# Optimization experiments

Hardware: AMD Instinct MI355X
Metric: run time of the kernel (lower is better)

The kernel has to match this reference:

```python
import jax, jax.numpy as jnp
import numpy as np

# --- module hyperparameters (init_kwargs) ---
IN_CH = 512
OUT_CH = 512
NUM_HEADS = 8
MODES = 64
LQ = 4096
LKV = 4096
E = IN_CH // NUM_HEADS      # per-head input dim = 64
EO = OUT_CH // NUM_HEADS    # per-head output dim = 64
B = 16

# mode_select_method='lowest' -> lowest-frequency modes, sorted (deterministic)
INDEX_Q = np.arange(min(MODES, LQ // 2))    # [Mq]
INDEX_KV = np.arange(min(MODES, LKV // 2))  # [Mkv]
SCALE = 1.0 / (IN_CH * OUT_CH)


def setup_inputs() -> dict:
    key = jax.random.key(0)
    kq, kk, kv, kw1, kw2 = jax.random.split(key, 5)
    return {
        "q": jax.random.normal(kq, (B, LQ, NUM_HEADS, E), jnp.float32),
        "k": jax.random.normal(kk, (B, LKV, NUM_HEADS, E), jnp.float32),
        "v": jax.random.normal(kv, (B, LKV, NUM_HEADS, E), jnp.float32),
        "weights1": SCALE * jax.random.normal(kw1, (NUM_HEADS, E, EO, len(INDEX_Q)), jnp.float32),
        "weights2": SCALE * jax.random.normal(kw2, (NUM_HEADS, E, EO, len(INDEX_Q)), jnp.float32),
    }


def reference(q, k, v, weights1, weights2):
    # q: [B, Lq, H, E]; k, v: [B, Lkv, H, E] (v is computed-but-unused in the
    # original forward; kept for signature fidelity).
    Bq, Lq, H, _ = q.shape
    xq = jnp.transpose(q, (0, 2, 3, 1))  # [B, H, E, Lq]
    xk = jnp.transpose(k, (0, 2, 3, 1))  # [B, H, E, Lkv]

    # rFFT along time, then gather the selected frequency modes
    xq_ft = jnp.fft.rfft(xq, axis=-1)[..., INDEX_Q]    # [B, H, E, Mq] complex
    xk_ft = jnp.fft.rfft(xk, axis=-1)[..., INDEX_KV]   # [B, H, E, Mkv] complex

    # complex cross-attention over modes (contract head-dim E)
    xqk = jnp.einsum('bhex,bhey->bhxy', xq_ft, xk_ft)  # [B, H, Mq, Mkv]
    # tanh applied independently to real/imag parts (as in compl activation)
    xqk = jax.lax.complex(jnp.tanh(xqk.real), jnp.tanh(xqk.imag))

    xqkv = jnp.einsum('bhxy,bhey->bhex', xqk, xk_ft)   # [B, H, E, Mq]

    w = jax.lax.complex(weights1, weights2)            # [H, E, EO, Mq]
    xqkvw = jnp.einsum('bhex,heox->bhox', xqkv, w)     # [B, H, EO, Mq]

    # scatter selected modes back into full half-spectrum, inverse FFT
    out_ft = jnp.zeros((Bq, H, EO, Lq // 2 + 1), jnp.complex64)
    out_ft = out_ft.at[..., INDEX_Q].set(xqkvw)
    out = jnp.fft.irfft(out_ft, n=Lq, axis=-1)         # [B, H, EO, Lq]

    out = jnp.transpose(out, (0, 3, 1, 2)) / (IN_CH * OUT_CH)  # [B, Lq, H, EO]
    return out
```

## Files before the change

### kernel.cpp

```cpp
#include <hip/hip_runtime.h>
#include <math.h>


constexpr float TWOPI_L = 1.5339807878856412e-3f;

typedef __attribute__((ext_vector_type(8))) short short8;
typedef __attribute__((ext_vector_type(4))) float f32x4;

__device__ __forceinline__ unsigned short f2bf(float f) {
    unsigned int u = __builtin_bit_cast(unsigned int, f);
    unsigned int r = (u + 0x7fffu + ((u >> 16) & 1u)) >> 16;
    return (unsigned short)r;
}
__device__ __forceinline__ float bf2f(unsigned short h) {
    unsigned int u = ((unsigned int)h) << 16;
    return __builtin_bit_cast(float, u);
}
__device__ __forceinline__ unsigned int cvtpk(float a, float b) {
    unsigned int r;
    asm("v_cvt_pk_bf16_f32 %0, %1, %2" : "=v"(r) : "v"(a), "v"(b));
    return r;
}
__device__ __forceinline__ void barrier_lds_only() {
    asm volatile("s_waitcnt lgkmcnt(0)\n\ts_barrier" ::: "memory");
}

__global__ __launch_bounds__(256) void k0_twiddle(unsigned short* __restrict__ Whi,
                                                  unsigned short* __restrict__ Wlo) {
    const int idx = blockIdx.x * 256 + threadIdx.x;
    const int kt = idx >> 9;
    const int rb = (idx >> 6) & 7;
    const int l15 = (idx >> 2) & 15;
    const int lg = idx & 3;
    const int r_tab = rb * 16 + l15;
    int m, c;
    if (r_tab < 64) { m = (r_tab >> 1) * 2;            c = r_tab & 1; }
    else            { m = (((r_tab - 64) >> 1) * 2) + 1; c = r_tab & 1; }
    const int addr = (kt * 8 + rb) * 512 + l15 * 32 + lg * 8;
    unsigned short hbuf[8], lbuf[8];
#pragma unroll
    for (int j = 0; j < 8; ++j) {
        const int t = kt * 32 + lg * 8 + j;
        float sv, cv;
        sincosf((float)((m * t) & 4095) * TWOPI_L, &sv, &cv);
        const float v = c ? -sv : cv;
        const unsigned short hi = f2bf(v);
        hbuf[j] = hi;
        lbuf[j] = f2bf(v - bf2f(hi));
    }
    *(uint4*)(Whi + addr) = *(uint4*)hbuf;
    *(uint4*)(Wlo + addr) = *(uint4*)lbuf;
}

__global__ __launch_bounds__(256) void k0_basis(unsigned short* __restrict__ basis) {
    const int idx = blockIdx.x * 256 + threadIdx.x;
    const int p0 = idx << 2;
    const int t = p0 >> 6;
    unsigned int pk[4];
#pragma unroll
    for (int j = 0; j < 4; ++j) {
        const int m = (p0 & 63) + j;
        float sv, cv;
        sincosf((float)((m * t) & 4095) * TWOPI_L, &sv, &cv);
        const float c = (m == 0) ? 1.0f : 2.0f * cv;
        const float s = (m == 0) ? 0.0f : -2.0f * sv;
        pk[j] = (unsigned int)f2bf(c) | ((unsigned int)f2bf(s) << 16);
    }
    *(uint4*)(basis + (size_t)t * 128u + ((p0 & 63) << 1)) =
        make_uint4(pk[0], pk[1], pk[2], pk[3]);
}

__global__ __launch_bounds__(256, 4) void k1_mfma(const float* __restrict__ q,
                                                  const float* __restrict__ kin,
                                                  const unsigned short* __restrict__ Whi,
                                                  const unsigned short* __restrict__ Wlo,
                                                  float* __restrict__ Xq, float* __restrict__ Xk,
                                                  float* __restrict__ Pq, float* __restrict__ Pk)
{
    __shared__ unsigned short xT[4][64][40];

    const int tid = threadIdx.x;
    const int bid = blockIdx.x;
    const int bh = bid >> 4, src = (bid >> 3) & 1, seg = bid & 7;
    const int b = bh >> 3, h = bh & 7;
    const float* __restrict__ x = src ? kin : q;
    const float* xb = x + (size_t)b * 2097152u + (size_t)h * 64u;

    const int fp = (tid & 15) * 2;
    const int e0s = (tid >> 4) * 4;

    const int wid = tid >> 6, lane = tid & 63;
    const int l15 = lane & 15, lg = lane >> 4;
    const int aoffL = l15 * 32 + lg * 8;
    const int sel = (wid >> 1) * 2;

    f32x4 acc[2][4];
#pragma unroll
    for (int mt = 0; mt < 2; ++mt)
#pragma unroll
        for (int nt = 0; nt < 4; ++nt)
            acc[mt][nt] = (f32x4){0.f, 0.f, 0.f, 0.f};

    for (int it = 0; it < 8; ++it) {
        const int t0 = seg * 256 + it * 32;
        float rs[16];
        {
            const float* r0 = xb + (size_t)(t0 + fp) * 512u + e0s;
            *(f32x4*)&rs[0]  = *(const f32x4*)r0;
            *(f32x4*)&rs[4]  = *(const f32x4*)(r0 + 512);
            *(f32x4*)&rs[8]  = *(const f32x4*)(r0 + 2048 * 512);
            *(f32x4*)&rs[12] = *(const f32x4*)(r0 + 2048 * 512 + 512);
        }
        short8 Ah[2], Al[2];
#pragma unroll
        for (int mt = 0; mt < 2; ++mt) {
            const size_t o = (size_t)(((seg * 8 + it) * 8 + (wid * 2 + mt)) * 512 + aoffL);
            Ah[mt] = *(const short8*)(Whi + o);
            Al[mt] = *(const short8*)(Wlo + o);
        }
#pragma unroll
        for (int ee = 0; ee < 4; ++ee) {
            const float a0 = rs[ee], a1 = rs[4 + ee];
            const float c0 = rs[8 + ee], c1 = rs[12 + ee];
            const float xp0 = a0 + c0, xp1 = a1 + c1;
            const float xm0 = a0 - c0, xm1 = a1 - c1;
            const int e = e0s + ee;
            const unsigned int php = cvtpk(xp0, xp1);
            const float ph0 = __builtin_bit_cast(float, php << 16);
            const float ph1 = __builtin_bit_cast(float, php & 0xffff0000u);
            const unsigned int plp = cvtpk(xp0 - ph0, xp1 - ph1);
            const unsigned int mhp = cvtpk(xm0, xm1);
            const float mh0 = __builtin_bit_cast(float, mhp << 16);
            const float mh1 = __builtin_bit_cast(float, mhp & 0xffff0000u);
            const unsigned int mlp = cvtpk(xm0 - mh0, xm1 - mh1);
            *(unsigned int*)&xT[0][e][fp] = php;
            *(unsigned int*)&xT[1][e][fp] = plp;
            *(unsigned int*)&xT[2][e][fp] = mhp;
            *(unsigned int*)&xT[3][e][fp] = mlp;
        }
        barrier_lds_only();

        const unsigned short* sh = &xT[sel][0][0];
        const unsigned short* sl = &xT[sel + 1][0][0];
#pragma unroll
        for (int nt = 0; nt < 4; ++nt) {
            const int ri = (nt * 16 + l15) * 40 + 8 * lg;
            const short8 Bh = *(const short8*)(sh + ri);
            const short8 Bl = *(const short8*)(sl + ri);
#pragma unroll
            for (int mt = 0; mt < 2; ++mt)
                acc[mt][nt] = __builtin_amdgcn_mfma_f32_16x16x32_bf16(Ah[mt], Bh, acc[mt][nt], 0, 0, 0);
#pragma unroll
            for (int mt = 0; mt < 2; ++mt)
                acc[mt][nt] = __builtin_amdgcn_mfma_f32_16x16x32_bf16(Ah[mt], Bl, acc[mt][nt], 0, 0, 0);
#pragma unroll
            for (int mt = 0; mt < 2; ++mt)
                acc[mt][nt] = __builtin_amdgcn_mfma_f32_16x16x32_bf16(Al[mt], Bh, acc[mt][nt], 0, 0, 0);
        }
        barrier_lds_only();
    }

    float* Xd;
    if (seg == 0) Xd = src ? Xk : Xq;
    else          Xd = (src ? Pk : Pq) + (size_t)(seg - 1) * 1048576u;
    Xd += (size_t)bh * 8192u;
    const int oddw = wid >> 1;
    const int wb = wid & 1;
#pragma unroll
    for (int mt = 0; mt < 2; ++mt) {
        const int r0 = (wb * 2 + mt) * 32 + 8 * lg + 2 * oddw;
#pragma unroll
        for (int nt = 0; nt < 4; ++nt) {
            const int e = nt * 16 + l15;
            *(float2*)(Xd + (size_t)e * 128u + r0) =
                make_float2(acc[mt][nt][0], acc[mt][nt][1]);
            *(float2*)(Xd + (size_t)e * 128u + r0 + 4) =
                make_float2(acc[mt][nt][2], acc[mt][nt][3]);
        }
    }
}

__global__ __launch_bounds__(256) void k1_reduce(float* __restrict__ Xq, const float* __restrict__ Pq,
                                                 float* __restrict__ Xk, const float* __restrict__ Pk) {
    const int i = blockIdx.x * 256 + threadIdx.x;
    float4* a = (float4*)Xq;
    float4* c = (float4*)Xk;
    float4 v = a[i], w = c[i];
#pragma unroll
    for (int s = 0; s < 7; ++s) {
        const float4 p = ((const float4*)(Pq + (size_t)s * 1048576u))[i];
        const float4 r = ((const float4*)(Pk + (size_t)s * 1048576u))[i];
        v.x += p.x; v.y += p.y; v.z += p.z; v.w += p.w;
        w.x += r.x; w.y += r.y; w.z += r.z; w.w += r.w;
    }
    a[i] = v;
    c[i] = w;
}

__global__ __launch_bounds__(256) void k2a_p1(const float* __restrict__ Xq,
                                              const float* __restrict__ Xk,
                                              float* __restrict__ P)
{
    const int blk = blockIdx.x;
    const int bh = blk >> 2, xt = blk & 3;
    __shared__ float sQ[64 * 32];
    __shared__ float sK[64 * 128];
    const int tid = threadIdx.x;
    const float* Xqb = Xq + (size_t)bh * 8192u;
    const float* Xkb = Xk + (size_t)bh * 8192u;

#pragma unroll
    for (int p = 0; p < 2; ++p) {
        const int f4 = tid + p * 256;
        const int row = f4 >> 3, c4 = f4 & 7;
        *(float4*)&sQ[row * 32 + c4 * 4] = *(const float4*)(Xqb + row * 128 + xt * 32 + c4 * 4);
    }
#pragma unroll
    for (int p = 0; p < 8; ++p) {
        const int f4 = tid + p * 256;
        *(float4*)&sK[f4 * 4] = *(const float4*)(Xkb + f4 * 4);
    }
    __syncthreads();

    const int xg = tid & 15, yg = tid >> 4;
    float aR[4] = {0.f, 0.f, 0.f, 0.f}, aI[4] = {0.f, 0.f, 0.f, 0.f};
#pragma unroll 8
    for (int e = 0; e < 64; ++e) {
        const float2 qv = *(const float2*)&sQ[e * 32 + 2 * xg];
        const float4 k0 = *(const float4*)&sK[e * 128 + 8 * yg];
        const float4 k1v = *(const float4*)&sK[e * 128 + 8 * yg + 4];
        aR[0] += qv.x * k0.x - qv.y * k0.y;   aI[0] += qv.x * k0.y + qv.y * k0.x;
        aR[1] += qv.x * k0.z - qv.y * k0.w;   aI[1] += qv.x * k0.w + qv.y * k0.z;
        aR[2] += qv.x * k1v.x - qv.y * k1v.y; aI[2] += qv.x * k1v.y + qv.y * k1v.x;
        aR[3] += qv.x * k1v.z - qv.y * k1v.w; aI[3] += qv.x * k1v.w + qv.y * k1v.z;
    }
    float* Pb = P + (size_t)bh * 8192u;
    const int x_abs = xt * 16 + xg;
#pragma unroll
    for (int j = 0; j < 4; ++j) {
        const int y = 4 * yg + j;
        *(float2*)(Pb + (size_t)y * 128u + 2 * x_abs) =
            make_float2(tanhf(aR[j]), tanhf(aI[j]));
    }
}

__global__ __launch_bounds__(256) void k2b_p3(const float* __restrict__ P,
                                              const float* __restrict__ Xk,
                                              float* __restrict__ PVG)
{
    const int blk = blockIdx.x;
    const int bh = blk >> 2, et = blk & 3;
    const int b = bh >> 3, h = bh & 7;
    __shared__ float sP[64 * 128];
    __shared__ float sKe[16 * 132];
    const int tid = threadIdx.x;
    const float* Pb = P + (size_t)bh * 8192u;
    const float* Xkb = Xk + (size_t)bh * 8192u + (size_t)(et * 16) * 128u;

#pragma unroll
    for (int p = 0; p < 8; ++p) {
        const int f4 = tid + p * 256;
        *(float4*)&sP[f4 * 4] = *(const float4*)(Pb + f4 * 4);
    }
#pragma unroll
    for (int p = 0; p < 2; ++p) {
        const int f4 = tid + p * 256;
        const int row = f4 >> 5, c4 = f4 & 31;
        *(float4*)&sKe[row * 132 + c4 * 4] = *(const float4*)(Xkb + row * 128 + c4 * 4);
    }
    __syncthreads();

    const int xg = tid & 15, el = tid >> 4;
    float aR[4] = {0.f, 0.f, 0.f, 0.f}, aI[4] = {0.f, 0.f, 0.f, 0.f};
#pragma unroll 8
    for (int y = 0; y < 64; ++y) {
        const float2 kv = *(const float2*)&sKe[el * 132 + 2 * y];
        const float4 p0 = *(const float4*)&sP[y * 128 + 8 * xg];
        const float4 p1 = *(const float4*)&sP[y * 128 + 8 * xg + 4];
        aR[0] += p0.x * kv.x - p0.y * kv.y;   aI[0] += p0.x * kv.y + p0.y * kv.x;
        aR[1] += p0.z * kv.x - p0.w * kv.y;   aI[1] += p0.z * kv.y + p0.w * kv.x;
        aR[2] += p1.x * kv.x - p1.y * kv.y;   aI[2] += p1.x * kv.y + p1.y * kv.x;
        aR[3] += p1.z * kv.x - p1.w * kv.y;   aI[3] += p1.z * kv.y + p1.w * kv.x;
    }
    const int e_abs = et * 16 + el;
    float* base = PVG + (size_t)h * 131072u;
#pragma unroll
    for (int j = 0; j < 4; ++j) {
        const int m = 4 * xg + j;
        base[(size_t)m * 2048u + 0u    + (size_t)b * 64u + e_abs] = aR[j];
        base[(size_t)m * 2048u + 1024u + (size_t)b * 64u + e_abs] = aI[j];
    }
}

__global__ __launch_bounds__(256) void kwt(const float* __restrict__ w1,
                                           const float* __restrict__ w2,
                                           float* __restrict__ wT)
{
    const int blk = blockIdx.x;
    const int h = blk >> 6, e = blk & 63;
    const int tid = threadIdx.x;
    const int m = tid & 63, oq = tid >> 6;
    const float* w1b = w1 + ((size_t)(h * 64 + e)) * 4096u;
    const float* w2b = w2 + ((size_t)(h * 64 + e)) * 4096u;
    float buf[32];
#pragma unroll
    for (int i = 0; i < 16; ++i) {
        const int o = oq * 16 + i;
        buf[2 * i]     = w1b[o * 64 + m];
        buf[2 * i + 1] = w2b[o * 64 + m];
    }
    float* dst = wT + (((size_t)(h * 64 + m)) * 64u + e) * 128u + oq * 32;
#pragma unroll
    for (int i = 0; i < 8; ++i)
        *(float4*)(dst + i * 4) = *(float4*)&buf[i * 4];
}

__global__ __launch_bounds__(256) void k2c_p4(const float* __restrict__ PVG,
                                              const float* __restrict__ wT,
                                              unsigned short* __restrict__ XWThi,
                                              unsigned short* __restrict__ XWTlo)
{
    const int blk = blockIdx.x;
    const int h = blk >> 6, m = blk & 63;
    __shared__ float sA[32 * 68];
    __shared__ float sW[64 * 128];
    const int tid = threadIdx.x;
    const float* Ab = PVG + (size_t)h * 131072u + (size_t)m * 2048u;
    const float* Wb = wT + ((size_t)h * 64u + m) * 8192u;

#pragma unroll
    for (int p = 0; p < 2; ++p) {
        const int f4 = tid + p * 256;
        const int row = f4 >> 4, e0 = (f4 & 15) * 4;
        *(float4*)&sA[row * 68 + e0] = *(const float4*)(Ab + row * 64 + e0);
    }
#pragma unroll
    for (int p = 0; p < 8; ++p) {
        const int f4 = tid + p * 256;
        *(float4*)&sW[f4 * 4] = *(const float4*)(Wb + f4 * 4);
    }
    __syncthreads();

    const int og = tid & 15, b = tid >> 4;
    float aR[4] = {0.f, 0.f, 0.f, 0.f}, aI[4] = {0.f, 0.f, 0.f, 0.f};
#pragma unroll 8
    for (int e = 0; e < 64; ++e) {
        const float pR = sA[b * 68 + e];
        const float pI = sA[(16 + b) * 68 + e];
        const float4 w0 = *(const float4*)&sW[e * 128 + 8 * og];
        const float4 w1v = *(const float4*)&sW[e * 128 + 8 * og + 4];
        aR[0] += pR * w0.x - pI * w0.y;   aI[0] += pR * w0.y + pI * w0.x;
        aR[1] += pR * w0.z - pI * w0.w;   aI[1] += pR * w0.w + pI * w0.z;
        aR[2] += pR * w1v.x - pI * w1v.y; aI[2] += pR * w1v.y + pI * w1v.x;
        aR[3] += pR * w1v.z - pI * w1v.w; aI[3] += pR * w1v.w + pI * w1v.z;
    }
    const int bh = b * 8 + h;
    unsigned short* Th = XWThi + (size_t)bh * 8192u;
    unsigned short* Tl = XWTlo + (size_t)bh * 8192u;
#pragma unroll
    for (int j = 0; j < 4; ++j) {
        const int o = 4 * og + j;
        const unsigned int hp = cvtpk(aR[j], aI[j]);
        const float hR = __builtin_bit_cast(float, hp << 16);
        const float hI = __builtin_bit_cast(float, hp & 0xffff0000u);
        const unsigned int lp = cvtpk(aR[j] - hR, aI[j] - hI);
        *(unsigned int*)(Th + (size_t)o * 128u + 2 * m) = hp;
        *(unsigned int*)(Tl + (size_t)o * 128u + 2 * m) = lp;
    }
}

__global__ __launch_bounds__(256, 3) void k3_mfma(const unsigned short* __restrict__ basis,
                                                  const unsigned short* __restrict__ XWThi,
                                                  const unsigned short* __restrict__ XWTlo,
                                                  float* __restrict__ out)
{
    const int bid = blockIdx.x;
    const int bh = bid >> 4, tc = bid & 15;
    const int b = bh >> 3, h = bh & 7;
    const int tid = threadIdx.x;
    const int wid = tid >> 6, lane = tid & 63;
    const int l15 = lane & 15, lg = lane >> 4;

    const int t0 = tc * 256 + wid * 64;
    const unsigned short* Th = XWThi + (size_t)bh * 8192u;
    const unsigned short* Tl = XWTlo + (size_t)bh * 8192u;

    f32x4 acc[4][4];
#pragma unroll
    for (int mt = 0; mt < 4; ++mt)
#pragma unroll
        for (int nt = 0; nt < 4; ++nt)
            acc[mt][nt] = (f32x4){0.f, 0.f, 0.f, 0.f};

#pragma unroll
    for (int ks = 0; ks < 4; ++ks) {
        const int ko = ks * 32 + 8 * lg;
        short8 A[4], Bh[4], Bl[4];
#pragma unroll
        for (int mt = 0; mt < 4; ++mt)
            A[mt] = *(const short8*)(basis + (size_t)(t0 + mt * 16 + l15) * 128u + ko);
#pragma unroll
        for (int nt = 0; nt < 4; ++nt) {
            Bh[nt] = *(const short8*)(Th + (size_t)(nt * 16 + l15) * 128u + ko);
            Bl[nt] = *(const short8*)(Tl + (size_t)(nt * 16 + l15) * 128u + ko);
        }
#pragma unroll
        for (int mt = 0; mt < 4; ++mt)
#pragma unroll
            for (int nt = 0; nt < 4; ++nt)
                acc[mt][nt] = __builtin_amdgcn_mfma_f32_16x16x32_bf16(A[mt], Bh[nt], acc[mt][nt], 0, 0, 0);
#pragma unroll
        for (int mt = 0; mt < 4; ++mt)
#pragma unroll
            for (int nt = 0; nt < 4; ++nt)
                acc[mt][nt] = __builtin_amdgcn_mfma_f32_16x16x32_bf16(A[mt], Bl[nt], acc[mt][nt], 0, 0, 0);
    }

    const float scale = 9.313225746154785e-10f;
#pragma unroll
    for (int mt = 0; mt < 4; ++mt)
#pragma unroll
        for (int nt = 0; nt < 4; ++nt) {
            const int o = nt * 16 + l15;
#pragma unroll
            for (int j = 0; j < 4; ++j) {
                const int t = t0 + mt * 16 + 4 * lg + j;
                out[((size_t)(b * 4096 + t) * 8u + (size_t)h) * 64u + o] = acc[mt][nt][j] * scale;
            }
        }
}

extern "C" void kernel_launch(void* const* d_in, const int* in_sizes, int n_in,
                              void* d_out, int out_size, void* d_ws, size_t ws_size,
                              hipStream_t stream) {
    (void)in_sizes; (void)n_in; (void)out_size; (void)ws_size;
    const float* q  = (const float*)d_in[0];
    const float* k  = (const float*)d_in[1];
    const float* w1 = (const float*)d_in[3];
    const float* w2 = (const float*)d_in[4];
    float* out = (float*)d_out;

    float* ws = (float*)d_ws;
    float* Xq = ws;
    float* Xk = ws + 1048576;
    unsigned short* XWThi = (unsigned short*)(ws + 2097152);
    unsigned short* XWTlo = XWThi + 1048576;
    unsigned short* basis = (unsigned short*)ws;

    unsigned short* Whi = (unsigned short*)out;
    unsigned short* Wlo = Whi + 262144;
    float* Pq  = out + 524288;
    float* Pk  = out + 7864320;
    float* P   = out + 16777216;
    float* wT  = out + 17825792;
    float* PVG = out + 22020096;

    hipLaunchKernelGGL(k0_twiddle, dim3(128),  dim3(256), 0, stream, Whi, Wlo);
    hipLaunchKernelGGL(k1_mfma,    dim3(2048), dim3(256), 0, stream, q, k, Whi, Wlo, Xq, Xk, Pq, Pk);
    hipLaunchKernelGGL(k1_reduce,  dim3(1024), dim3(256), 0, stream, Xq, Pq, Xk, Pk);
    hipLaunchKernelGGL(k2a_p1,     dim3(512),  dim3(256), 0, stream, Xq, Xk, P);
    hipLaunchKernelGGL(k0_basis,   dim3(256),  dim3(256), 0, stream, basis);
    hipLaunchKernelGGL(k2b_p3,     dim3(512),  dim3(256), 0, stream, P, Xk, PVG);
    hipLaunchKernelGGL(kwt,        dim3(512),  dim3(256), 0, stream, w1, w2, wT);
    hipLaunchKernelGGL(k2c_p4,     dim3(512),  dim3(256), 0, stream, PVG, wT, XWThi, XWTlo);
    hipLaunchKernelGGL(k3_mfma,    dim3(2048), dim3(256), 0, stream, basis, XWThi, XWTlo, out);
}
```

Measured before the change: 231.3 us.

## Build MFMA input fragments in registers, drop LDS transpose in forward DFT

The forward-DFT MFMA kernel now loads the signal directly into A-operand fragments in registers, with each wave owning 16 channels. This removes the LDS staging buffer and its two barriers per iteration. The twiddle table layout is reordered to serve as the B operand, and the time axis is split into 4 segments instead of 8, which halves the grid and the number of partial sums to reduce. In exchange, the global loads become strided scalar reads (8 per operand per lane) and the output is written with scalar stores instead of float2.

```diff
diff --git a/kernel.cpp b/kernel.cpp
--- a/kernel.cpp
+++ b/kernel.cpp
@@ -21,26 +21,33 @@
     asm("v_cvt_pk_bf16_f32 %0, %1, %2" : "=v"(r) : "v"(a), "v"(b));
     return r;
 }
-__device__ __forceinline__ void barrier_lds_only() {
-    asm volatile("s_waitcnt lgkmcnt(0)\n\ts_barrier" ::: "memory");
+__device__ __forceinline__ void mk_frag(const float* v, short8& hi, short8& lo) {
+    unsigned int hp[4], lp[4];
+#pragma unroll
+    for (int p = 0; p < 4; ++p) {
+        hp[p] = cvtpk(v[2 * p], v[2 * p + 1]);
+        const float h0 = __builtin_bit_cast(float, hp[p] << 16);
+        const float h1 = __builtin_bit_cast(float, hp[p] & 0xffff0000u);
+        lp[p] = cvtpk(v[2 * p] - h0, v[2 * p + 1] - h1);
+    }
+    hi = __builtin_bit_cast(short8, *(uint4*)hp);
+    lo = __builtin_bit_cast(short8, *(uint4*)lp);
 }
 
 __global__ __launch_bounds__(256) void k0_twiddle(unsigned short* __restrict__ Whi,
                                                   unsigned short* __restrict__ Wlo) {
     const int idx = blockIdx.x * 256 + threadIdx.x;
-    const int kt = idx >> 9;
-    const int rb = (idx >> 6) & 7;
-    const int l15 = (idx >> 2) & 15;
-    const int lg = idx & 3;
-    const int r_tab = rb * 16 + l15;
-    int m, c;
-    if (r_tab < 64) { m = (r_tab >> 1) * 2;            c = r_tab & 1; }
-    else            { m = (((r_tab - 64) >> 1) * 2) + 1; c = r_tab & 1; }
-    const int addr = (kt * 8 + rb) * 512 + l15 * 32 + lg * 8;
+    const int ksg = idx >> 9;
+    const int r = (idx >> 2) & 127;
+    const int ttg = idx & 3;
+    const int nt = r >> 4, l15 = r & 15;
+    const int m = 2 * (8 * (nt & 3) + (l15 >> 1)) + (nt >> 2);
+    const int c = l15 & 1;
+    const int addr = (ksg * 128 + r) * 32 + ttg * 8;
     unsigned short hbuf[8], lbuf[8];
 #pragma unroll
     for (int j = 0; j < 8; ++j) {
-        const int t = kt * 32 + lg * 8 + j;
+        const int t = ksg * 32 + ttg * 8 + j;
         float sv, cv;
         sincosf((float)((m * t) & 4095) * TWOPI_L, &sv, &cv);
         const float v = c ? -sv : cv;
@@ -77,105 +84,64 @@
                                                   float* __restrict__ Xq, float* __restrict__ Xk,
                                                   float* __restrict__ Pq, float* __restrict__ Pk)
 {
-    __shared__ unsigned short xT[4][64][40];
-
     const int tid = threadIdx.x;
     const int bid = blockIdx.x;
-    const int bh = bid >> 4, src = (bid >> 3) & 1, seg = bid & 7;
+    const int bh = bid >> 3, src = (bid >> 2) & 1, seg = bid & 3;
     const int b = bh >> 3, h = bh & 7;
     const float* __restrict__ x = src ? kin : q;
     const float* xb = x + (size_t)b * 2097152u + (size_t)h * 64u;
 
-    const int fp = (tid & 15) * 2;
-    const int e0s = (tid >> 4) * 4;
-
     const int wid = tid >> 6, lane = tid & 63;
     const int l15 = lane & 15, lg = lane >> 4;
-    const int aoffL = l15 * 32 + lg * 8;
-    const int sel = (wid >> 1) * 2;
-
-    f32x4 acc[2][4];
-#pragma unroll
-    for (int mt = 0; mt < 2; ++mt)
-#pragma unroll
-        for (int nt = 0; nt < 4; ++nt)
-            acc[mt][nt] = (f32x4){0.f, 0.f, 0.f, 0.f};
-
-    for (int it = 0; it < 8; ++it) {
-        const int t0 = seg * 256 + it * 32;
-        float rs[16];
-        {
-            const float* r0 = xb + (size_t)(t0 + fp) * 512u + e0s;
-            *(f32x4*)&rs[0]  = *(const f32x4*)r0;
-            *(f32x4*)&rs[4]  = *(const f32x4*)(r0 + 512);
-            *(f32x4*)&rs[8]  = *(const f32x4*)(r0 + 2048 * 512);
-            *(f32x4*)&rs[12] = *(const f32x4*)(r0 + 2048 * 512 + 512);
+    const int ew = 16 * wid;
+    const float* xl = xb + (size_t)(ew + l15);
+
+    f32x4 acc[8];
+#pragma unroll
+    for (int nt = 0; nt < 8; ++nt) acc[nt] = (f32x4){0.f, 0.f, 0.f, 0.f};
+
+#pragma unroll 2
+    for (int ks = 0; ks < 16; ++ks) {
+        const int ksg = seg * 16 + ks;
+        const int t0 = ksg * 32 + 8 * lg;
+        float a[8], c[8];
+#pragma unroll
+        for (int j = 0; j < 8; ++j) a[j] = xl[(size_t)(t0 + j) * 512u];
+#pragma unroll
+        for (int j = 0; j < 8; ++j) c[j] = xl[(size_t)(t0 + j + 2048) * 512u];
+        float xp[8], xm[8];
+#pragma unroll
+        for (int j = 0; j < 8; ++j) { xp[j] = a[j] + c[j]; xm[j] = a[j] - c[j]; }
+        short8 Ahp, Alp, Ahm, Alm;
+        mk_frag(xp, Ahp, Alp);
+        mk_frag(xm, Ahm, Alm);
+        const unsigned short* Wb = Whi + (size_t)(ksg * 128) * 32u + (size_t)(8 * lg);
+        const unsigned short* Wl = Wlo + (size_t)(ksg * 128) * 32u + (size_t)(8 * lg);
+#pragma unroll
+        for (int nt = 0; nt < 8; ++nt) {
+            const size_t ro = (size_t)((nt * 16 + l15) * 32);
+            const short8 Bh = *(const short8*)(Wb + ro);
+            const short8 Bl = *(const short8*)(Wl + ro);
+            const short8 Ah = (nt < 4) ? Ahp : Ahm;
+            const short8 Al = (nt < 4) ? Alp : Alm;
+            acc[nt] = __builtin_amdgcn_mfma_f32_16x16x32_bf16(Ah, Bh, acc[nt], 0, 0, 0);
+            acc[nt] = __builtin_amdgcn_mfma_f32_16x16x32_bf16(Ah, Bl, acc[nt], 0, 0, 0);
+            acc[nt] = __builtin_amdgcn_mfma_f32_16x16x32_bf16(Al, Bh, acc[nt], 0, 0, 0);
         }
-        short8 Ah[2], Al[2];
-#pragma unroll
-        for (int mt = 0; mt < 2; ++mt) {
-            const size_t o = (size_t)(((seg * 8 + it) * 8 + (wid * 2 + mt)) * 512 + aoffL);
-            Ah[mt] = *(const short8*)(Whi + o);
-            Al[mt] = *(const short8*)(Wlo + o);
-        }
-#pragma unroll
-        for (int ee = 0; ee < 4; ++ee) {
-            const float a0 = rs[ee], a1 = rs[4 + ee];
-            const float c0 = rs[8 + ee], c1 = rs[12 + ee];
-            const float xp0 = a0 + c0, xp1 = a1 + c1;
-            const float xm0 = a0 - c0, xm1 = a1 - c1;
-            const int e = e0s + ee;
-            const unsigned int php = cvtpk(xp0, xp1);
-            const float ph0 = __builtin_bit_cast(float, php << 16);
-            const float ph1 = __builtin_bit_cast(float, php & 0xffff0000u);
-            const unsigned int plp = cvtpk(xp0 - ph0, xp1 - ph1);
-            const unsigned int mhp = cvtpk(xm0, xm1);
-            const float mh0 = __builtin_bit_cast(float, mhp << 16);
-            const float mh1 = __builtin_bit_cast(float, mhp & 0xffff0000u);
-            const unsigned int mlp = cvtpk(xm0 - mh0, xm1 - mh1);
-            *(unsigned int*)&xT[0][e][fp] = php;
-            *(unsigned int*)&xT[1][e][fp] = plp;
-            *(unsigned int*)&xT[2][e][fp] = mhp;
-            *(unsigned int*)&xT[3][e][fp] = mlp;
-        }
-        barrier_lds_only();
-
-        const unsigned short* sh = &xT[sel][0][0];
-        const unsigned short* sl = &xT[sel + 1][0][0];
-#pragma unroll
-        for (int nt = 0; nt < 4; ++nt) {
-            const int ri = (nt * 16 + l15) * 40 + 8 * lg;
-            const short8 Bh = *(const short8*)(sh + ri);
-            const short8 Bl = *(const short8*)(sl + ri);
-#pragma unroll
-            for (int mt = 0; mt < 2; ++mt)
-                acc[mt][nt] = __builtin_amdgcn_mfma_f32_16x16x32_bf16(Ah[mt], Bh, acc[mt][nt], 0, 0, 0);
-#pragma unroll
-            for (int mt = 0; mt < 2; ++mt)
-                acc[mt][nt] = __builtin_amdgcn_mfma_f32_16x16x32_bf16(Ah[mt], Bl, acc[mt][nt], 0, 0, 0);
-#pragma unroll
-            for (int mt = 0; mt < 2; ++mt)
-                acc[mt][nt] = __builtin_amdgcn_mfma_f32_16x16x32_bf16(Al[mt], Bh, acc[mt][nt], 0, 0, 0);
-        }
-        barrier_lds_only();
     }
 
     float* Xd;
     if (seg == 0) Xd = src ? Xk : Xq;
     else          Xd = (src ? Pk : Pq) + (size_t)(seg - 1) * 1048576u;
     Xd += (size_t)bh * 8192u;
-    const int oddw = wid >> 1;
-    const int wb = wid & 1;
-#pragma unroll
-    for (int mt = 0; mt < 2; ++mt) {
-        const int r0 = (wb * 2 + mt) * 32 + 8 * lg + 2 * oddw;
-#pragma unroll
-        for (int nt = 0; nt < 4; ++nt) {
-            const int e = nt * 16 + l15;
-            *(float2*)(Xd + (size_t)e * 128u + r0) =
-                make_float2(acc[mt][nt][0], acc[mt][nt][1]);
-            *(float2*)(Xd + (size_t)e * 128u + r0 + 4) =
-                make_float2(acc[mt][nt][2], acc[mt][nt][3]);
+    const int col_base = 4 * (l15 >> 1) + (l15 & 1);
+#pragma unroll
+    for (int nt = 0; nt < 8; ++nt) {
+        const int col = 32 * (nt & 3) + 2 * (nt >> 2) + col_base;
+#pragma unroll
+        for (int reg = 0; reg < 4; ++reg) {
+            const int e = ew + 4 * lg + reg;
+            Xd[(size_t)e * 128u + col] = acc[nt][reg];
         }
     }
 }
@@ -187,7 +153,7 @@
     float4* c = (float4*)Xk;
     float4 v = a[i], w = c[i];
 #pragma unroll
-    for (int s = 0; s < 7; ++s) {
+    for (int s = 0; s < 3; ++s) {
         const float4 p = ((const float4*)(Pq + (size_t)s * 1048576u))[i];
         const float4 r = ((const float4*)(Pk + (size_t)s * 1048576u))[i];
         v.x += p.x; v.y += p.y; v.z += p.z; v.w += p.w;
@@ -450,13 +416,13 @@
     unsigned short* Whi = (unsigned short*)out;
     unsigned short* Wlo = Whi + 262144;
     float* Pq  = out + 524288;
-    float* Pk  = out + 7864320;
+    float* Pk  = out + 3670016;
     float* P   = out + 16777216;
     float* wT  = out + 17825792;
     float* PVG = out + 22020096;
 
     hipLaunchKernelGGL(k0_twiddle, dim3(128),  dim3(256), 0, stream, Whi, Wlo);
-    hipLaunchKernelGGL(k1_mfma,    dim3(2048), dim3(256), 0, stream, q, k, Whi, Wlo, Xq, Xk, Pq, Pk);
+    hipLaunchKernelGGL(k1_mfma,    dim3(1024), dim3(256), 0, stream, q, k, Whi, Wlo, Xq, Xk, Pq, Pk);
     hipLaunchKernelGGL(k1_reduce,  dim3(1024), dim3(256), 0, stream, Xq, Pq, Xk, Pk);
     hipLaunchKernelGGL(k2a_p1,     dim3(512),  dim3(256), 0, stream, Xq, Xk, P);
     hipLaunchKernelGGL(k0_basis,   dim3(256),  dim3(256), 0, stream, basis);
```

After: 242.2 us. 4.7% more time.

## Double-buffer k1 input loads via global_load_lds with swizzled LDS and fewer segments

Applied to the files above, without the earlier changes.

The forward DFT kernel now stages raw q/k rows into a double-buffered, XOR-swizzled LDS tile with direct global-to-LDS loads, prefetching the next time tile while the current one is converted to bf16 hi/lo and fed to MFMA. Each block also covers 512 time steps instead of 256, which halves the grid and the partial buffers, and the reduce kernel sums 3 partials instead of 7. This hides global load latency and cuts partial-sum traffic, at the cost of more LDS per block, lower target occupancy (launch bounds 3), and fewer blocks in flight.

```diff
diff --git a/kernel.cpp b/kernel.cpp
--- a/kernel.cpp
+++ b/kernel.cpp
@@ -21,9 +21,13 @@
     asm("v_cvt_pk_bf16_f32 %0, %1, %2" : "=v"(r) : "v"(a), "v"(b));
     return r;
 }
-__device__ __forceinline__ void barrier_lds_only() {
-    asm volatile("s_waitcnt lgkmcnt(0)\n\ts_barrier" ::: "memory");
-}
+__device__ __forceinline__ void gld16(const float* g, void* l) {
+    __builtin_amdgcn_global_load_lds(
+        (const __attribute__((address_space(1))) void*)(g),
+        (__attribute__((address_space(3))) void*)(l),
+        16, 0, 0);
+}
+#define MSKR(r) (((((r) & 7)) << 1) | ((((r) >> 3)) & 1))
 
 __global__ __launch_bounds__(256) void k0_twiddle(unsigned short* __restrict__ Whi,
                                                   unsigned short* __restrict__ Wlo) {
@@ -34,7 +38,7 @@
     const int lg = idx & 3;
     const int r_tab = rb * 16 + l15;
     int m, c;
-    if (r_tab < 64) { m = (r_tab >> 1) * 2;            c = r_tab & 1; }
+    if (r_tab < 64) { m = (r_tab >> 1) * 2;              c = r_tab & 1; }
     else            { m = (((r_tab - 64) >> 1) * 2) + 1; c = r_tab & 1; }
     const int addr = (kt * 8 + rb) * 512 + l15 * 32 + lg * 8;
     unsigned short hbuf[8], lbuf[8];
@@ -70,28 +74,27 @@
         make_uint4(pk[0], pk[1], pk[2], pk[3]);
 }
 
-__global__ __launch_bounds__(256, 4) void k1_mfma(const float* __restrict__ q,
+__global__ __launch_bounds__(256, 3) void k1_mfma(const float* __restrict__ q,
                                                   const float* __restrict__ kin,
                                                   const unsigned short* __restrict__ Whi,
                                                   const unsigned short* __restrict__ Wlo,
                                                   float* __restrict__ Xq, float* __restrict__ Xk,
                                                   float* __restrict__ Pq, float* __restrict__ Pk)
 {
+    __shared__ float raw[2][64][64];
     __shared__ unsigned short xT[4][64][40];
 
     const int tid = threadIdx.x;
     const int bid = blockIdx.x;
-    const int bh = bid >> 4, src = (bid >> 3) & 1, seg = bid & 7;
+    const int bh = bid >> 3, src = (bid >> 2) & 1, seg = bid & 3;
     const int b = bh >> 3, h = bh & 7;
     const float* __restrict__ x = src ? kin : q;
     const float* xb = x + (size_t)b * 2097152u + (size_t)h * 64u;
 
-    const int fp = (tid & 15) * 2;
-    const int e0s = (tid >> 4) * 4;
-
     const int wid = tid >> 6, lane = tid & 63;
     const int l15 = lane & 15, lg = lane >> 4;
-    const int aoffL = l15 * 32 + lg * 8;
+    const int fp = (tid & 15) * 2;
+    const int eqs = tid >> 4;
     const int sel = (wid >> 1) * 2;
 
     f32x4 acc[2][4];
@@ -101,64 +104,87 @@
         for (int nt = 0; nt < 4; ++nt)
             acc[mt][nt] = (f32x4){0.f, 0.f, 0.f, 0.f};
 
-    for (int it = 0; it < 8; ++it) {
-        const int t0 = seg * 256 + it * 32;
-        float rs[16];
-        {
-            const float* r0 = xb + (size_t)(t0 + fp) * 512u + e0s;
-            *(f32x4*)&rs[0]  = *(const f32x4*)r0;
-            *(f32x4*)&rs[4]  = *(const f32x4*)(r0 + 512);
-            *(f32x4*)&rs[8]  = *(const f32x4*)(r0 + 2048 * 512);
-            *(f32x4*)&rs[12] = *(const f32x4*)(r0 + 2048 * 512 + 512);
-        }
-        short8 Ah[2], Al[2];
-#pragma unroll
-        for (int mt = 0; mt < 2; ++mt) {
-            const size_t o = (size_t)(((seg * 8 + it) * 8 + (wid * 2 + mt)) * 512 + aoffL);
-            Ah[mt] = *(const short8*)(Whi + o);
-            Al[mt] = *(const short8*)(Wlo + o);
-        }
-#pragma unroll
-        for (int ee = 0; ee < 4; ++ee) {
-            const float a0 = rs[ee], a1 = rs[4 + ee];
-            const float c0 = rs[8 + ee], c1 = rs[12 + ee];
-            const float xp0 = a0 + c0, xp1 = a1 + c1;
-            const float xm0 = a0 - c0, xm1 = a1 - c1;
-            const int e = e0s + ee;
-            const unsigned int php = cvtpk(xp0, xp1);
-            const float ph0 = __builtin_bit_cast(float, php << 16);
-            const float ph1 = __builtin_bit_cast(float, php & 0xffff0000u);
-            const unsigned int plp = cvtpk(xp0 - ph0, xp1 - ph1);
-            const unsigned int mhp = cvtpk(xm0, xm1);
-            const float mh0 = __builtin_bit_cast(float, mhp << 16);
-            const float mh1 = __builtin_bit_cast(float, mhp & 0xffff0000u);
-            const unsigned int mlp = cvtpk(xm0 - mh0, xm1 - mh1);
-            *(unsigned int*)&xT[0][e][fp] = php;
-            *(unsigned int*)&xT[1][e][fp] = plp;
-            *(unsigned int*)&xT[2][e][fp] = mhp;
-            *(unsigned int*)&xT[3][e][fp] = mlp;
-        }
-        barrier_lds_only();
-
-        const unsigned short* sh = &xT[sel][0][0];
-        const unsigned short* sl = &xT[sel + 1][0][0];
-#pragma unroll
-        for (int nt = 0; nt < 4; ++nt) {
-            const int ri = (nt * 16 + l15) * 40 + 8 * lg;
-            const short8 Bh = *(const short8*)(sh + ri);
-            const short8 Bl = *(const short8*)(sl + ri);
-#pragma unroll
-            for (int mt = 0; mt < 2; ++mt)
-                acc[mt][nt] = __builtin_amdgcn_mfma_f32_16x16x32_bf16(Ah[mt], Bh, acc[mt][nt], 0, 0, 0);
-#pragma unroll
-            for (int mt = 0; mt < 2; ++mt)
-                acc[mt][nt] = __builtin_amdgcn_mfma_f32_16x16x32_bf16(Ah[mt], Bl, acc[mt][nt], 0, 0, 0);
-#pragma unroll
-            for (int mt = 0; mt < 2; ++mt)
-                acc[mt][nt] = __builtin_amdgcn_mfma_f32_16x16x32_bf16(Al[mt], Bh, acc[mt][nt], 0, 0, 0);
-        }
-        barrier_lds_only();
-    }
+#define K1_STAGE(IT, NXT) do {                                                  \
+    const int t0_ = (seg * 16 + (IT)) * 32;                                     \
+    _Pragma("unroll")                                                           \
+    for (int j = 0; j < 4; ++j) {                                               \
+        const int c_ = wid * 4 + j;                                             \
+        const int rl_ = 4 * c_ + (lane >> 4);                                   \
+        const int t_ = t0_ + (rl_ & 31) + ((rl_ >> 5) << 11);                   \
+        const int sq_ = (lane & 15) ^ MSKR(rl_);                                \
+        gld16(xb + (size_t)t_ * 512u + (size_t)(sq_ * 4), &raw[NXT][c_ * 4][0]); \
+    }                                                                           \
+} while (0)
+
+#define K1_TILE(IT, CUR, STAGE_STMT, VMC) do {                                  \
+    short8 Ah[2], Al[2];                                                        \
+    const int ksg_ = seg * 16 + (IT);                                           \
+    _Pragma("unroll")                                                           \
+    for (int mt = 0; mt < 2; ++mt) {                                            \
+        const size_t o_ = (size_t)((ksg_ * 8 + (wid * 2 + mt)) * 512 + l15 * 32 + lg * 8); \
+        Ah[mt] = *(const short8*)(Whi + o_);                                    \
+        Al[mt] = *(const short8*)(Wlo + o_);                                    \
+    }                                                                           \
+    __builtin_amdgcn_sched_barrier(0);    \
+    STAGE_STMT;                                                                 \
+    asm volatile("s_waitcnt vmcnt(" #VMC ")\n\ts_barrier" ::: "memory");        \
+    {           \
+        float rs[16];                                                           \
+        *(f32x4*)&rs[0]  = *(const f32x4*)&raw[CUR][fp     ][(eqs ^ MSKR(fp))      * 4]; \
+        *(f32x4*)&rs[4]  = *(const f32x4*)&raw[CUR][fp + 1 ][(eqs ^ MSKR(fp + 1))  * 4]; \
+        *(f32x4*)&rs[8]  = *(const f32x4*)&raw[CUR][fp + 32][(eqs ^ MSKR(fp + 32)) * 4]; \
+        *(f32x4*)&rs[12] = *(const f32x4*)&raw[CUR][fp + 33][(eqs ^ MSKR(fp + 33)) * 4]; \
+        _Pragma("unroll")                                                       \
+        for (int ee = 0; ee < 4; ++ee) {                                        \
+            const float a0 = rs[ee], a1 = rs[4 + ee];                           \
+            const float c0 = rs[8 + ee], c1 = rs[12 + ee];                      \
+            const float xp0 = a0 + c0, xp1 = a1 + c1;                           \
+            const float xm0 = a0 - c0, xm1 = a1 - c1;                           \
+            const int e_ = eqs * 4 + ee;                                        \
+            const unsigned int php = cvtpk(xp0, xp1);                           \
+            const float ph0 = __builtin_bit_cast(float, php << 16);             \
+            const float ph1 = __builtin_bit_cast(float, php & 0xffff0000u);     \
+            const unsigned int plp = cvtpk(xp0 - ph0, xp1 - ph1);               \
+            const unsigned int mhp = cvtpk(xm0, xm1);                           \
+            const float mh0 = __builtin_bit_cast(float, mhp << 16);             \
+            const float mh1 = __builtin_bit_cast(float, mhp & 0xffff0000u);     \
+            const unsigned int mlp = cvtpk(xm0 - mh0, xm1 - mh1);               \
+            *(unsigned int*)&xT[0][e_][fp] = php;                               \
+            *(unsigned int*)&xT[1][e_][fp] = plp;                               \
+            *(unsigned int*)&xT[2][e_][fp] = mhp;                               \
+            *(unsigned int*)&xT[3][e_][fp] = mlp;                               \
+        }                                                                       \
+    }                                                                           \
+    asm volatile("s_waitcnt lgkmcnt(0)\n\ts_barrier" ::: "memory");             \
+    {             \
+        const unsigned short* sh = &xT[sel][0][0];                              \
+        const unsigned short* sl = &xT[sel + 1][0][0];                          \
+        _Pragma("unroll")                                                       \
+        for (int nt = 0; nt < 4; ++nt) {                                        \
+            const int ri = (nt * 16 + l15) * 40 + 8 * lg;                       \
+            const short8 Bh = *(const short8*)(sh + ri);                        \
+            const short8 Bl = *(const short8*)(sl + ri);                        \
+            _Pragma("unroll")                                                   \
+            for (int mt = 0; mt < 2; ++mt)                                      \
+                acc[mt][nt] = __builtin_amdgcn_mfma_f32_16x16x32_bf16(Ah[mt], Bh, acc[mt][nt], 0, 0, 0); \
+            _Pragma("unroll")                                                   \
+            for (int mt = 0; mt < 2; ++mt)                                      \
+                acc[mt][nt] = __builtin_amdgcn_mfma_f32_16x16x32_bf16(Ah[mt], Bl, acc[mt][nt], 0, 0, 0); \
+            _Pragma("unroll")                                                   \
+            for (int mt = 0; mt < 2; ++mt)                                      \
+                acc[mt][nt] = __builtin_amdgcn_mfma_f32_16x16x32_bf16(Al[mt], Bh, acc[mt][nt], 0, 0, 0); \
+        }                                                                       \
+    }                                                                           \
+} while (0)
+
+    K1_STAGE(0, 0);
+    for (int it = 0; it < 15; ++it) {
+        K1_TILE(it, (it & 1), K1_STAGE(it + 1, (it + 1) & 1), 8);
+    }
+    K1_TILE(15, 1, (void)0, 4);
+
+#undef K1_TILE
+#undef K1_STAGE
 
     float* Xd;
     if (seg == 0) Xd = src ? Xk : Xq;
@@ -187,7 +213,7 @@
     float4* c = (float4*)Xk;
     float4 v = a[i], w = c[i];
 #pragma unroll
-    for (int s = 0; s < 7; ++s) {
+    for (int s = 0; s < 3; ++s) {
         const float4 p = ((const float4*)(Pq + (size_t)s * 1048576u))[i];
         const float4 r = ((const float4*)(Pk + (size_t)s * 1048576u))[i];
         v.x += p.x; v.y += p.y; v.z += p.z; v.w += p.w;
@@ -450,13 +476,13 @@
     unsigned short* Whi = (unsigned short*)out;
     unsigned short* Wlo = Whi + 262144;
     float* Pq  = out + 524288;
-    float* Pk  = out + 7864320;
+    float* Pk  = out + 3670016;
     float* P   = out + 16777216;
     float* wT  = out + 17825792;
     float* PVG = out + 22020096;
 
     hipLaunchKernelGGL(k0_twiddle, dim3(128),  dim3(256), 0, stream, Whi, Wlo);
-    hipLaunchKernelGGL(k1_mfma,    dim3(2048), dim3(256), 0, stream, q, k, Whi, Wlo, Xq, Xk, Pq, Pk);
+    hipLaunchKernelGGL(k1_mfma,    dim3(1024), dim3(256), 0, stream, q, k, Whi, Wlo, Xq, Xk, Pq, Pk);
     hipLaunchKernelGGL(k1_reduce,  dim3(1024), dim3(256), 0, stream, Xq, Pq, Xk, Pk);
     hipLaunchKernelGGL(k2a_p1,     dim3(512),  dim3(256), 0, stream, Xq, Xk, P);
     hipLaunchKernelGGL(k0_basis,   dim3(256),  dim3(256), 0, stream, basis);
```

Result: faster. 213.1 us (-7.9%).
